# Kernel tuning notes

Hardware: AMD Instinct MI355X
Metric: run time of the kernel (lower is better)

Reference implementation:

```python
import jax, jax.numpy as jnp
import numpy as np

D_MODEL = 1024
D_STATE = 64


def setup_inputs() -> dict:
    key = jax.random.key(0)
    k_x, k_a, k_b, k_c, k_d = jax.random.split(key, 5)
    x = jax.random.normal(k_x, (4, 4096, D_MODEL), dtype=jnp.float32)
    # parameter init mirrors _init_parameters
    A_diag = jax.random.uniform(k_a, (D_STATE,), minval=-0.5, maxval=0.5, dtype=jnp.float32)
    def xavier(k, shape):
        fan_in, fan_out = shape
        limit = float(np.sqrt(6.0 / (fan_in + fan_out)))
        return jax.random.uniform(k, shape, minval=-limit, maxval=limit, dtype=jnp.float32)
    B = xavier(k_b, (D_MODEL, D_STATE))
    C = xavier(k_c, (D_STATE, D_MODEL))
    D = xavier(k_d, (D_MODEL, D_MODEL)) * 0.1
    return {"x": x, "A_diag": A_diag, "B": B, "C": C, "D": D}


def reference(x, A_diag, B, C, D):
    # h_t = sigmoid(A_diag) * h_{t-1} + x_t @ B ; y_t = h_t @ C + x_t @ D
    # dropout is identity in eval mode.
    a = jax.nn.sigmoid(A_diag)                      # [S_state]
    u = jnp.einsum('btd,ds->bts', x, B)             # precompute input drive [B,T,S]

    def step(h, u_t):                               # h: [B,S], u_t: [B,S]
        h = a * h + u_t
        return h, h

    h0 = jnp.zeros((x.shape[0], A_diag.shape[0]), dtype=x.dtype)
    _, hs = jax.lax.scan(step, h0, jnp.swapaxes(u, 0, 1))  # hs: [T,B,S]
    hs = jnp.swapaxes(hs, 0, 1)                            # [B,T,S]
    y = jnp.einsum('bts,sd->btd', hs, C) + jnp.einsum('btd,de->bte', x, D)
    return y
```

## Files before the change

kernel.cpp:

```cpp
#include <hip/hip_runtime.h>
#include <hip/hip_bf16.h>

using bf16x8 = __attribute__((ext_vector_type(8))) __bf16;
using f32x4  = __attribute__((ext_vector_type(4))) float;

#define MTOT   16384
#define DMODEL 1024
#define DSTATE 64
#define KBIG   1088

__device__ __forceinline__ ushort f2b(float f) {
  __hip_bfloat16 h = __float2bfloat16(f);
  return *reinterpret_cast<ushort*>(&h);
}

__device__ __forceinline__ void gld_lds16(const ushort* g, const char* l) {
  using gptr_t = const __attribute__((address_space(1))) uint32_t*;
  using lptr_t = __attribute__((address_space(3))) uint32_t*;
  __builtin_amdgcn_global_load_lds(
      reinterpret_cast<gptr_t>(reinterpret_cast<uintptr_t>(g)),
      reinterpret_cast<lptr_t>(static_cast<uint32_t>(reinterpret_cast<uintptr_t>(l))),
      16, 0, 0);
}

#define BARRIER() do { asm volatile("" ::: "memory"); __builtin_amdgcn_s_barrier(); asm volatile("" ::: "memory"); } while (0)
#define VMCNT4() asm volatile("s_waitcnt vmcnt(4)" ::: "memory")
#define VMCNT0() asm volatile("s_waitcnt vmcnt(0)" ::: "memory")

__global__ __launch_bounds__(256) void prep_wb(const float* __restrict__ A_diag,
    const float* __restrict__ B, const float* __restrict__ C, const float* __restrict__ D,
    ushort* __restrict__ Wt, ushort* __restrict__ Btu, float* __restrict__ aSig) {
  __shared__ float tile[64][65];
  int bid = blockIdx.x;
  int tid = threadIdx.x;
  int r = tid >> 2;
  if (bid < 272) {
    int bk = bid % 17, bn = bid / 17;
    int k0 = bk * 64, n0 = bn * 64;
    const float* srow = (k0 + r < DSTATE)
        ? (C + (size_t)(k0 + r) * DMODEL + n0)
        : (D + (size_t)(k0 + r - DSTATE) * DMODEL + n0);
#pragma unroll
    for (int it = 0; it < 4; ++it) {
      int c4 = (tid & 3) + it * 4;
      float4 v = *reinterpret_cast<const float4*>(srow + c4 * 4);
      tile[r][c4 * 4 + 0] = v.x; tile[r][c4 * 4 + 1] = v.y;
      tile[r][c4 * 4 + 2] = v.z; tile[r][c4 * 4 + 3] = v.w;
    }
    __syncthreads();
#pragma unroll
    for (int it = 0; it < 2; ++it) {
      int gq = (tid & 3) + it * 4;
      ushort o[8];
#pragma unroll
      for (int j = 0; j < 8; ++j) o[j] = f2b(tile[gq * 8 + j][r]);
      *reinterpret_cast<uint4*>(&Wt[(size_t)(n0 + r) * KBIG + k0 + gq * 8]) =
          *reinterpret_cast<uint4*>(o);
    }
  } else {
    int k0 = (bid - 272) * 64;
    const float* srow = B + (size_t)(k0 + r) * DSTATE;
#pragma unroll
    for (int it = 0; it < 4; ++it) {
      int c4 = (tid & 3) + it * 4;
      float4 v = *reinterpret_cast<const float4*>(srow + c4 * 4);
      tile[r][c4 * 4 + 0] = v.x; tile[r][c4 * 4 + 1] = v.y;
      tile[r][c4 * 4 + 2] = v.z; tile[r][c4 * 4 + 3] = v.w;
    }
    __syncthreads();
#pragma unroll
    for (int it = 0; it < 2; ++it) {
      int gq = (tid & 3) + it * 4;
      ushort o[8];
#pragma unroll
      for (int j = 0; j < 8; ++j) o[j] = f2b(tile[gq * 8 + j][r]);
      *reinterpret_cast<uint4*>(&Btu[(size_t)r * DMODEL + k0 + gq * 8]) =
          *reinterpret_cast<uint4*>(o);
    }
    if (bid == 272 && tid < DSTATE) aSig[tid] = 1.0f / (1.0f + expf(-A_diag[tid]));
  }
}

__global__ __launch_bounds__(256) void fused_xu(const float* __restrict__ x,
    const ushort* __restrict__ Btu, const float* __restrict__ aSig,
    ushort* __restrict__ Z, float* __restrict__ Uloc, float* __restrict__ carry) {
  __shared__ ushort As[64][136];
  __shared__ float  Ul[64][68];
  int tid = threadIdx.x;
  int w = tid >> 6, lane = tid & 63;
  int l16 = lane & 15, lh = lane >> 4;
  int row0 = blockIdx.x * 64;

  f32x4 acc[4] = {};
  float4 xv[4][2];
#pragma unroll
  for (int p = 0; p < 4; ++p) {
    int fi = p * 256 + tid;
    int r = fi >> 4, kq = fi & 15;
    const float* src = x + (size_t)(row0 + r) * 1024 + kq * 8;
    xv[p][0] = *reinterpret_cast<const float4*>(src);
    xv[p][1] = *reinterpret_cast<const float4*>(src + 4);
  }
  for (int c = 0; c < 8; ++c) {
    int k0 = c * 128;
#pragma unroll
    for (int p = 0; p < 4; ++p) {
      int fi = p * 256 + tid;
      int r = fi >> 4, kq = fi & 15;
      ushort o[8] = {f2b(xv[p][0].x), f2b(xv[p][0].y), f2b(xv[p][0].z), f2b(xv[p][0].w),
                     f2b(xv[p][1].x), f2b(xv[p][1].y), f2b(xv[p][1].z), f2b(xv[p][1].w)};
      uint4 pk = *reinterpret_cast<uint4*>(o);
      *reinterpret_cast<uint4*>(&Z[(size_t)(row0 + r) * KBIG + DSTATE + k0 + kq * 8]) = pk;
      *reinterpret_cast<uint4*>(&As[r][kq * 8]) = pk;
    }
    __syncthreads();
    if (c < 7) {
      int k1 = k0 + 128;
#pragma unroll
      for (int p = 0; p < 4; ++p) {
        int fi = p * 256 + tid;
        int r = fi >> 4, kq = fi & 15;
        const float* src = x + (size_t)(row0 + r) * 1024 + k1 + kq * 8;
        xv[p][0] = *reinterpret_cast<const float4*>(src);
        xv[p][1] = *reinterpret_cast<const float4*>(src + 4);
      }
    }
#pragma unroll
    for (int ks = 0; ks < 4; ++ks) {
      bf16x8 af = *reinterpret_cast<const bf16x8*>(&As[w * 16 + l16][ks * 32 + lh * 8]);
#pragma unroll
      for (int n = 0; n < 4; ++n) {
        bf16x8 bf = *reinterpret_cast<const bf16x8*>(
            &Btu[(size_t)(n * 16 + l16) * 1024 + k0 + ks * 32 + lh * 8]);
        acc[n] = __builtin_amdgcn_mfma_f32_16x16x32_bf16(af, bf, acc[n], 0, 0, 0);
      }
    }
    __syncthreads();
  }
#pragma unroll
  for (int n = 0; n < 4; ++n)
#pragma unroll
    for (int j = 0; j < 4; ++j)
      Ul[w * 16 + lh * 4 + j][n * 16 + l16] = acc[n][j];
  __syncthreads();
  int s = lane;
  float as = aSig[s];
  float h = 0.0f;
  int g = blockIdx.x * 4 + w;
#pragma unroll
  for (int i = 0; i < 16; ++i) {
    h = fmaf(as, h, Ul[w * 16 + i][s]);
    Uloc[(size_t)(g * 16 + i) * 64 + s] = h;
  }
  carry[(size_t)g * 64 + s] = h;
}

__global__ __launch_bounds__(256) void scan_fix2(const float* __restrict__ aSig,
    const float* __restrict__ Uloc, const float* __restrict__ carry,
    ushort* __restrict__ Z) {
  int w = threadIdx.x >> 6, s = threadIdx.x & 63;
  int g = blockIdx.x * 4 + w;
  int b = g >> 8, c = g & 255;
  float as = aSig[s];
  float aL = as;
#pragma unroll
  for (int q = 0; q < 4; ++q) aL *= aL;
  const float* cb = carry + ((size_t)b << 8) * 64 + s;
  float H = 0.0f;
  for (int c0 = 0; c0 < 256; c0 += 16) {
    if (c0 >= c) break;
    float v[16];
#pragma unroll
    for (int i = 0; i < 16; ++i) v[i] = cb[(size_t)(c0 + i) * 64];
#pragma unroll
    for (int i = 0; i < 16; ++i)
      if (c0 + i < c) H = fmaf(aL, H, v[i]);
  }
  float p = as;
  size_t ubase = (size_t)g * 16 * 64 + s;
  size_t zbase = (size_t)(g * 16) * KBIG + s;
#pragma unroll
  for (int i = 0; i < 16; ++i) {
    float h = fmaf(p, H, Uloc[ubase + (size_t)i * 64]);
    p *= as;
    Z[zbase + (size_t)i * KBIG] = f2b(h);
  }
}

__global__ __launch_bounds__(512) void gemm256(const ushort* __restrict__ A, int lda,
                                               const ushort* __restrict__ Bt, int ldb,
                                               float* __restrict__ Cc, int ldc, int K) {
  extern __shared__ __align__(128) char smem[];
  const int tid = threadIdx.x;
  const int wid = tid >> 6, lane = tid & 63;
  const int wm = wid >> 2, wn = wid & 3;
  const int l16 = lane & 15, lh = lane >> 4;

  int bid = blockIdx.x;
  int swz = (bid & 7) * ((int)gridDim.x >> 3) + (bid >> 3);
  const int bmRow = (swz >> 2) * 256;
  const int bnCol = (swz & 3) * 256;

  const int NT = K / 64;

  const int cswz = ((lh ^ (l16 & 7)) << 4);
  const int sRow = lane >> 3;
  const int sCol = (((lane & 7) ^ (lane >> 3)) << 3);

  f32x4 acc[8][4] = {};
  bf16x8 aR[8], bR[8];

  auto stageA = [&](int buf, int t, int h) {
    size_t r = (size_t)(bmRow + h * 128 + wid * 8 + sRow);
    const ushort* g0 = A + r * (size_t)lda + t * 64 + sCol;
    const char* d = smem + buf * 65536 + (h * 128 + wid * 8) * 128;
    gld_lds16(g0, d);
    gld_lds16(g0 + (size_t)64 * lda, d + 64 * 128);
  };
  auto stageB = [&](int buf, int t, int h) {
    size_t r = (size_t)(bnCol + h * 128 + wid * 8 + sRow);
    const ushort* g0 = Bt + r * (size_t)ldb + t * 64 + sCol;
    const char* d = smem + buf * 65536 + 32768 + (h * 128 + wid * 8) * 128;
    gld_lds16(g0, d);
    gld_lds16(g0 + (size_t)64 * ldb, d + 64 * 128);
  };
  auto loadA = [&](int buf, int qm) {
#pragma unroll
    for (int m = 0; m < 4; ++m)
#pragma unroll
      for (int ks = 0; ks < 2; ++ks)
        aR[m * 2 + ks] = *reinterpret_cast<const bf16x8*>(
            smem + buf * 65536 + (wm * 128 + qm * 64 + m * 16 + l16) * 128 + (cswz ^ (ks * 64)));
  };
  auto loadB = [&](int buf, int qn) {
#pragma unroll
    for (int n = 0; n < 2; ++n)
#pragma unroll
      for (int ks = 0; ks < 2; ++ks)
        bR[qn * 4 + n * 2 + ks] = *reinterpret_cast<const bf16x8*>(
            smem + buf * 65536 + 32768 + (wn * 64 + qn * 32 + n * 16 + l16) * 128 + (cswz ^ (ks * 64)));
  };
  auto mfmaQ = [&](int qm, int qn) {
    __builtin_amdgcn_s_setprio(1);
    __builtin_amdgcn_sched_barrier(0);
#pragma unroll
    for (int ks = 0; ks < 2; ++ks)
#pragma unroll
      for (int m = 0; m < 4; ++m)
#pragma unroll
        for (int n = 0; n < 2; ++n)
          acc[qm * 4 + m][qn * 2 + n] = __builtin_amdgcn_mfma_f32_16x16x32_bf16(
              aR[m * 2 + ks], bR[qn * 4 + n * 2 + ks], acc[qm * 4 + m][qn * 2 + n], 0, 0, 0);
    __builtin_amdgcn_sched_barrier(0);
    __builtin_amdgcn_s_setprio(0);
  };

  stageA(0, 0, 0); stageA(0, 0, 1); stageB(0, 0, 0); stageB(0, 0, 1);
  if (1 < NT) { stageA(1, 1, 0); stageA(1, 1, 1); stageB(1, 1, 0); stageB(1, 1, 1); }
  VMCNT0();
  BARRIER();

  for (int t = 0; t < NT; t += 2) {
    const bool s01 = (t > 0) && (t + 1 < NT);
    const bool s23 = (t + 2 < NT);
    const bool s67 = (t + 3 < NT);
    loadA(0, 0); loadB(0, 0);
    if (s01) stageA(1, t + 1, 0);
    BARRIER(); mfmaQ(0, 0); BARRIER();
    loadB(0, 1);
    if (s01) stageA(1, t + 1, 1);
    BARRIER(); mfmaQ(0, 1); BARRIER();
    loadA(0, 1);
    if (s23) stageB(0, t + 2, 0);
    BARRIER(); mfmaQ(1, 0); BARRIER();
    if (s23) stageB(0, t + 2, 1);
    BARRIER(); mfmaQ(1, 1);
    if (s23) { VMCNT4(); } else { VMCNT0(); }
    BARRIER();
    if (t + 1 < NT) {
      loadA(1, 0); loadB(1, 0);
      if (s23) stageA(0, t + 2, 0);
      BARRIER(); mfmaQ(0, 0); BARRIER();
      loadB(1, 1);
      if (s23) stageA(0, t + 2, 1);
      BARRIER(); mfmaQ(0, 1); BARRIER();
      loadA(1, 1);
      if (s67) stageB(1, t + 3, 0);
      BARRIER(); mfmaQ(1, 0); BARRIER();
      if (s67) stageB(1, t + 3, 1);
      BARRIER(); mfmaQ(1, 1);
      if (s67) { VMCNT4(); } else { VMCNT0(); }
      BARRIER();
    }
  }

#pragma unroll
  for (int i = 0; i < 8; ++i)
#pragma unroll
    for (int jn = 0; jn < 4; ++jn)
#pragma unroll
      for (int j = 0; j < 4; ++j) {
        int r = bmRow + wm * 128 + (i >> 2) * 64 + (i & 3) * 16 + lh * 4 + j;
        int c = bnCol + wn * 64 + (jn >> 1) * 32 + (jn & 1) * 16 + l16;
        Cc[(size_t)r * ldc + c] = acc[i][jn][j];
      }
}

extern "C" void kernel_launch(void* const* d_in, const int* in_sizes, int n_in,
                              void* d_out, int out_size, void* d_ws, size_t ws_size,
                              hipStream_t stream) {
  const float* x      = (const float*)d_in[0];
  const float* A_diag = (const float*)d_in[1];
  const float* B      = (const float*)d_in[2];
  const float* C      = (const float*)d_in[3];
  const float* D      = (const float*)d_in[4];
  float* y = (float*)d_out;

  char* w = (char*)d_ws;
  ushort* Z     = (ushort*)(w);
  ushort* Wt    = (ushort*)(w + 35651584);
  ushort* Btu   = (ushort*)(w + 37879808);
  float*  Uloc  = (float*) (w + 38010880);
  float*  carry = (float*) (w + 42205184);
  float*  aSig  = (float*) (w + 42467328);

  (void)hipFuncSetAttribute(reinterpret_cast<const void*>(&gemm256),
                            hipFuncAttributeMaxDynamicSharedMemorySize, 131072);

  prep_wb<<<dim3(288), dim3(256), 0, stream>>>(A_diag, B, C, D, Wt, Btu, aSig);
  fused_xu<<<dim3(256), dim3(256), 0, stream>>>(x, Btu, aSig, Z, Uloc, carry);
  scan_fix2<<<dim3(256), dim3(256), 0, stream>>>(aSig, Uloc, carry, Z);
  gemm256<<<dim3(64 * 4), dim3(512), 131072, stream>>>(Z, KBIG, Wt, KBIG, y, DMODEL, KBIG);
}
```

Measured before the change: 84.85 us.

## Fuse weight prep, input projection and chunked scan into one cooperative kernel

Merges the three pre-GEMM kernels (weight transpose/convert, x@B with local scan, and scan fix-up) into a single cooperative kernel that uses grid-wide syncs between phases. Local chunk states stay in shared memory across the second grid sync, so the Uloc global round trip is removed. The intent is to cut two kernel launch gaps and the Uloc write and read traffic. In exchange it relies on cooperative launch with all 256 blocks co-resident and adds grid-barrier overhead.

```diff
diff --git a/kernel.cpp b/kernel.cpp
--- a/kernel.cpp
+++ b/kernel.cpp
@@ -1,5 +1,8 @@
 #include <hip/hip_runtime.h>
 #include <hip/hip_bf16.h>
+#include <hip/hip_cooperative_groups.h>
+
+namespace cg = cooperative_groups;
 
 using bf16x8 = __attribute__((ext_vector_type(8))) __bf16;
 using f32x4  = __attribute__((ext_vector_type(4))) float;
@@ -27,163 +30,162 @@
 #define VMCNT4() asm volatile("s_waitcnt vmcnt(4)" ::: "memory")
 #define VMCNT0() asm volatile("s_waitcnt vmcnt(0)" ::: "memory")
 
-__global__ __launch_bounds__(256) void prep_wb(const float* __restrict__ A_diag,
-    const float* __restrict__ B, const float* __restrict__ C, const float* __restrict__ D,
-    ushort* __restrict__ Wt, ushort* __restrict__ Btu, float* __restrict__ aSig) {
-  __shared__ float tile[64][65];
-  int bid = blockIdx.x;
-  int tid = threadIdx.x;
-  int r = tid >> 2;
-  if (bid < 272) {
-    int bk = bid % 17, bn = bid / 17;
-    int k0 = bk * 64, n0 = bn * 64;
-    const float* srow = (k0 + r < DSTATE)
-        ? (C + (size_t)(k0 + r) * DMODEL + n0)
-        : (D + (size_t)(k0 + r - DSTATE) * DMODEL + n0);
-#pragma unroll
-    for (int it = 0; it < 4; ++it) {
-      int c4 = (tid & 3) + it * 4;
-      float4 v = *reinterpret_cast<const float4*>(srow + c4 * 4);
-      tile[r][c4 * 4 + 0] = v.x; tile[r][c4 * 4 + 1] = v.y;
-      tile[r][c4 * 4 + 2] = v.z; tile[r][c4 * 4 + 3] = v.w;
-    }
-    __syncthreads();
-#pragma unroll
-    for (int it = 0; it < 2; ++it) {
-      int gq = (tid & 3) + it * 4;
-      ushort o[8];
-#pragma unroll
-      for (int j = 0; j < 8; ++j) o[j] = f2b(tile[gq * 8 + j][r]);
-      *reinterpret_cast<uint4*>(&Wt[(size_t)(n0 + r) * KBIG + k0 + gq * 8]) =
-          *reinterpret_cast<uint4*>(o);
-    }
-  } else {
-    int k0 = (bid - 272) * 64;
-    const float* srow = B + (size_t)(k0 + r) * DSTATE;
-#pragma unroll
-    for (int it = 0; it < 4; ++it) {
-      int c4 = (tid & 3) + it * 4;
-      float4 v = *reinterpret_cast<const float4*>(srow + c4 * 4);
-      tile[r][c4 * 4 + 0] = v.x; tile[r][c4 * 4 + 1] = v.y;
-      tile[r][c4 * 4 + 2] = v.z; tile[r][c4 * 4 + 3] = v.w;
-    }
-    __syncthreads();
-#pragma unroll
-    for (int it = 0; it < 2; ++it) {
-      int gq = (tid & 3) + it * 4;
-      ushort o[8];
-#pragma unroll
-      for (int j = 0; j < 8; ++j) o[j] = f2b(tile[gq * 8 + j][r]);
-      *reinterpret_cast<uint4*>(&Btu[(size_t)r * DMODEL + k0 + gq * 8]) =
-          *reinterpret_cast<uint4*>(o);
-    }
-    if (bid == 272 && tid < DSTATE) aSig[tid] = 1.0f / (1.0f + expf(-A_diag[tid]));
+__global__ __launch_bounds__(256) void mega(const float* __restrict__ x,
+    const float* __restrict__ A_diag, const float* __restrict__ B,
+    const float* __restrict__ C, const float* __restrict__ D,
+    ushort* __restrict__ Wt, ushort* __restrict__ Btu, float* __restrict__ aSig,
+    ushort* __restrict__ Z, float* __restrict__ carry) {
+  __shared__ __align__(16) char smem_u[34816];
+  float  (*tile)[65] = reinterpret_cast<float(*)[65]>(smem_u);
+  ushort (*As)[136]  = reinterpret_cast<ushort(*)[136]>(smem_u);
+  float  (*Ul)[68]   = reinterpret_cast<float(*)[68]>(smem_u + 17408);
+
+  const int tid = threadIdx.x;
+  const int w = tid >> 6, lane = tid & 63;
+  const int l16 = lane & 15, lh = lane >> 4;
+
+  if (blockIdx.x == 0 && tid < DSTATE) aSig[tid] = 1.0f / (1.0f + expf(-A_diag[tid]));
+  {
+    int r = tid >> 2;
+    for (int job = blockIdx.x; job < 288; job += 256) {
+      if (job < 272) {
+        int bk = job % 17, bn = job / 17;
+        int k0 = bk * 64, n0 = bn * 64;
+        const float* srow = (k0 + r < DSTATE)
+            ? (C + (size_t)(k0 + r) * DMODEL + n0)
+            : (D + (size_t)(k0 + r - DSTATE) * DMODEL + n0);
+#pragma unroll
+        for (int it = 0; it < 4; ++it) {
+          int c4 = (tid & 3) + it * 4;
+          float4 v = *reinterpret_cast<const float4*>(srow + c4 * 4);
+          tile[r][c4 * 4 + 0] = v.x; tile[r][c4 * 4 + 1] = v.y;
+          tile[r][c4 * 4 + 2] = v.z; tile[r][c4 * 4 + 3] = v.w;
+        }
+        __syncthreads();
+#pragma unroll
+        for (int it = 0; it < 2; ++it) {
+          int gq = (tid & 3) + it * 4;
+          ushort o[8];
+#pragma unroll
+          for (int j = 0; j < 8; ++j) o[j] = f2b(tile[gq * 8 + j][r]);
+          *reinterpret_cast<uint4*>(&Wt[(size_t)(n0 + r) * KBIG + k0 + gq * 8]) =
+              *reinterpret_cast<uint4*>(o);
+        }
+      } else {
+        int k0 = (job - 272) * 64;
+        const float* srow = B + (size_t)(k0 + r) * DSTATE;
+#pragma unroll
+        for (int it = 0; it < 4; ++it) {
+          int c4 = (tid & 3) + it * 4;
+          float4 v = *reinterpret_cast<const float4*>(srow + c4 * 4);
+          tile[r][c4 * 4 + 0] = v.x; tile[r][c4 * 4 + 1] = v.y;
+          tile[r][c4 * 4 + 2] = v.z; tile[r][c4 * 4 + 3] = v.w;
+        }
+        __syncthreads();
+#pragma unroll
+        for (int it = 0; it < 2; ++it) {
+          int gq = (tid & 3) + it * 4;
+          ushort o[8];
+#pragma unroll
+          for (int j = 0; j < 8; ++j) o[j] = f2b(tile[gq * 8 + j][r]);
+          *reinterpret_cast<uint4*>(&Btu[(size_t)r * DMODEL + k0 + gq * 8]) =
+              *reinterpret_cast<uint4*>(o);
+        }
+      }
+      __syncthreads();
+    }
   }
-}
-
-__global__ __launch_bounds__(256) void fused_xu(const float* __restrict__ x,
-    const ushort* __restrict__ Btu, const float* __restrict__ aSig,
-    ushort* __restrict__ Z, float* __restrict__ Uloc, float* __restrict__ carry) {
-  __shared__ ushort As[64][136];
-  __shared__ float  Ul[64][68];
-  int tid = threadIdx.x;
-  int w = tid >> 6, lane = tid & 63;
-  int l16 = lane & 15, lh = lane >> 4;
-  int row0 = blockIdx.x * 64;
-
-  f32x4 acc[4] = {};
-  float4 xv[4][2];
-#pragma unroll
-  for (int p = 0; p < 4; ++p) {
-    int fi = p * 256 + tid;
-    int r = fi >> 4, kq = fi & 15;
-    const float* src = x + (size_t)(row0 + r) * 1024 + kq * 8;
-    xv[p][0] = *reinterpret_cast<const float4*>(src);
-    xv[p][1] = *reinterpret_cast<const float4*>(src + 4);
-  }
-  for (int c = 0; c < 8; ++c) {
-    int k0 = c * 128;
+
+  cg::this_grid().sync();
+
+  const int row0 = blockIdx.x * 64;
+  const int g = blockIdx.x * 4 + w;
+  {
+    f32x4 acc[4] = {};
+    float4 xv[4][2];
 #pragma unroll
     for (int p = 0; p < 4; ++p) {
       int fi = p * 256 + tid;
       int r = fi >> 4, kq = fi & 15;
-      ushort o[8] = {f2b(xv[p][0].x), f2b(xv[p][0].y), f2b(xv[p][0].z), f2b(xv[p][0].w),
-                     f2b(xv[p][1].x), f2b(xv[p][1].y), f2b(xv[p][1].z), f2b(xv[p][1].w)};
-      uint4 pk = *reinterpret_cast<uint4*>(o);
-      *reinterpret_cast<uint4*>(&Z[(size_t)(row0 + r) * KBIG + DSTATE + k0 + kq * 8]) = pk;
-      *reinterpret_cast<uint4*>(&As[r][kq * 8]) = pk;
-    }
-    __syncthreads();
-    if (c < 7) {
-      int k1 = k0 + 128;
+      const float* src = x + (size_t)(row0 + r) * 1024 + kq * 8;
+      xv[p][0] = *reinterpret_cast<const float4*>(src);
+      xv[p][1] = *reinterpret_cast<const float4*>(src + 4);
+    }
+    for (int c = 0; c < 8; ++c) {
+      int k0 = c * 128;
 #pragma unroll
       for (int p = 0; p < 4; ++p) {
         int fi = p * 256 + tid;
         int r = fi >> 4, kq = fi & 15;
-        const float* src = x + (size_t)(row0 + r) * 1024 + k1 + kq * 8;
-        xv[p][0] = *reinterpret_cast<const float4*>(src);
-        xv[p][1] = *reinterpret_cast<const float4*>(src + 4);
-      }
-    }
-#pragma unroll
-    for (int ks = 0; ks < 4; ++ks) {
-      bf16x8 af = *reinterpret_cast<const bf16x8*>(&As[w * 16 + l16][ks * 32 + lh * 8]);
-#pragma unroll
-      for (int n = 0; n < 4; ++n) {
-        bf16x8 bf = *reinterpret_cast<const bf16x8*>(
-            &Btu[(size_t)(n * 16 + l16) * 1024 + k0 + ks * 32 + lh * 8]);
-        acc[n] = __builtin_amdgcn_mfma_f32_16x16x32_bf16(af, bf, acc[n], 0, 0, 0);
-      }
-    }
-    __syncthreads();
+        ushort o[8] = {f2b(xv[p][0].x), f2b(xv[p][0].y), f2b(xv[p][0].z), f2b(xv[p][0].w),
+                       f2b(xv[p][1].x), f2b(xv[p][1].y), f2b(xv[p][1].z), f2b(xv[p][1].w)};
+        uint4 pk = *reinterpret_cast<uint4*>(o);
+        *reinterpret_cast<uint4*>(&Z[(size_t)(row0 + r) * KBIG + DSTATE + k0 + kq * 8]) = pk;
+        *reinterpret_cast<uint4*>(&As[r][kq * 8]) = pk;
+      }
+      __syncthreads();
+      if (c < 7) {
+        int k1 = k0 + 128;
+#pragma unroll
+        for (int p = 0; p < 4; ++p) {
+          int fi = p * 256 + tid;
+          int r = fi >> 4, kq = fi & 15;
+          const float* src = x + (size_t)(row0 + r) * 1024 + k1 + kq * 8;
+          xv[p][0] = *reinterpret_cast<const float4*>(src);
+          xv[p][1] = *reinterpret_cast<const float4*>(src + 4);
+        }
+      }
+#pragma unroll
+      for (int ks = 0; ks < 4; ++ks) {
+        bf16x8 af = *reinterpret_cast<const bf16x8*>(&As[w * 16 + l16][ks * 32 + lh * 8]);
+#pragma unroll
+        for (int n = 0; n < 4; ++n) {
+          bf16x8 bf = *reinterpret_cast<const bf16x8*>(
+              &Btu[(size_t)(n * 16 + l16) * 1024 + k0 + ks * 32 + lh * 8]);
+          acc[n] = __builtin_amdgcn_mfma_f32_16x16x32_bf16(af, bf, acc[n], 0, 0, 0);
+        }
+      }
+      __syncthreads();
+    }
+#pragma unroll
+    for (int n = 0; n < 4; ++n)
+#pragma unroll
+      for (int j = 0; j < 4; ++j)
+        Ul[w * 16 + lh * 4 + j][n * 16 + l16] = acc[n][j];
+    float as = aSig[lane];
+    float h = 0.0f;
+#pragma unroll
+    for (int i = 0; i < 16; ++i) h = fmaf(as, h, Ul[w * 16 + i][lane]);
+    carry[(size_t)g * 64 + lane] = h;
   }
-#pragma unroll
-  for (int n = 0; n < 4; ++n)
-#pragma unroll
-    for (int j = 0; j < 4; ++j)
-      Ul[w * 16 + lh * 4 + j][n * 16 + l16] = acc[n][j];
-  __syncthreads();
-  int s = lane;
-  float as = aSig[s];
-  float h = 0.0f;
-  int g = blockIdx.x * 4 + w;
-#pragma unroll
-  for (int i = 0; i < 16; ++i) {
-    h = fmaf(as, h, Ul[w * 16 + i][s]);
-    Uloc[(size_t)(g * 16 + i) * 64 + s] = h;
-  }
-  carry[(size_t)g * 64 + s] = h;
-}
-
-__global__ __launch_bounds__(256) void scan_fix2(const float* __restrict__ aSig,
-    const float* __restrict__ Uloc, const float* __restrict__ carry,
-    ushort* __restrict__ Z) {
-  int w = threadIdx.x >> 6, s = threadIdx.x & 63;
-  int g = blockIdx.x * 4 + w;
-  int b = g >> 8, c = g & 255;
-  float as = aSig[s];
-  float aL = as;
-#pragma unroll
-  for (int q = 0; q < 4; ++q) aL *= aL;
-  const float* cb = carry + ((size_t)b << 8) * 64 + s;
-  float H = 0.0f;
-  for (int c0 = 0; c0 < 256; c0 += 16) {
-    if (c0 >= c) break;
-    float v[16];
-#pragma unroll
-    for (int i = 0; i < 16; ++i) v[i] = cb[(size_t)(c0 + i) * 64];
-#pragma unroll
-    for (int i = 0; i < 16; ++i)
-      if (c0 + i < c) H = fmaf(aL, H, v[i]);
-  }
-  float p = as;
-  size_t ubase = (size_t)g * 16 * 64 + s;
-  size_t zbase = (size_t)(g * 16) * KBIG + s;
-#pragma unroll
-  for (int i = 0; i < 16; ++i) {
-    float h = fmaf(p, H, Uloc[ubase + (size_t)i * 64]);
-    p *= as;
-    Z[zbase + (size_t)i * KBIG] = f2b(h);
+
+  __threadfence();
+  cg::this_grid().sync();
+
+  {
+    int b = g >> 8, c = g & 255;
+    float as = aSig[lane];
+    float aL = as;
+#pragma unroll
+    for (int q = 0; q < 4; ++q) aL *= aL;
+    const float* cb = carry + ((size_t)b << 8) * 64 + lane;
+    float H = 0.0f;
+    for (int c0 = 0; c0 < 256; c0 += 16) {
+      if (c0 >= c) break;
+      float v[16];
+#pragma unroll
+      for (int i = 0; i < 16; ++i) v[i] = cb[(size_t)(c0 + i) * 64];
+#pragma unroll
+      for (int i = 0; i < 16; ++i)
+        if (c0 + i < c) H = fmaf(aL, H, v[i]);
+    }
+    float h = H;
+    size_t zbase = (size_t)(g * 16) * KBIG + lane;
+#pragma unroll
+    for (int i = 0; i < 16; ++i) {
+      h = fmaf(as, h, Ul[w * 16 + i][lane]);
+      Z[zbase + (size_t)i * KBIG] = f2b(h);
+    }
   }
 }
 
@@ -320,15 +322,15 @@
   ushort* Z     = (ushort*)(w);
   ushort* Wt    = (ushort*)(w + 35651584);
   ushort* Btu   = (ushort*)(w + 37879808);
-  float*  Uloc  = (float*) (w + 38010880);
-  float*  carry = (float*) (w + 42205184);
-  float*  aSig  = (float*) (w + 42467328);
+  float*  carry = (float*) (w + 38010880);
+  float*  aSig  = (float*) (w + 38273024);
 
   (void)hipFuncSetAttribute(reinterpret_cast<const void*>(&gemm256),
                             hipFuncAttributeMaxDynamicSharedMemorySize, 131072);
 
-  prep_wb<<<dim3(288), dim3(256), 0, stream>>>(A_diag, B, C, D, Wt, Btu, aSig);
-  fused_xu<<<dim3(256), dim3(256), 0, stream>>>(x, Btu, aSig, Z, Uloc, carry);
-  scan_fix2<<<dim3(256), dim3(256), 0, stream>>>(aSig, Uloc, carry, Z);
+  void* args[] = {(void*)&x, (void*)&A_diag, (void*)&B, (void*)&C, (void*)&D,
+                  (void*)&Wt, (void*)&Btu, (void*)&aSig, (void*)&Z, (void*)&carry};
+  (void)hipLaunchCooperativeKernel(reinterpret_cast<void*>(&mega),
+                                   dim3(256), dim3(256), args, 0, stream);
   gemm256<<<dim3(64 * 4), dim3(512), 131072, stream>>>(Z, KBIG, Wt, KBIG, y, DMODEL, KBIG);
 }
```

Result: slower. 182.2 us (+114.8%).

## Replace 256x256 GEMM tile with 128x128 tile and simpler double-buffered loop

Applied to the files above, without the earlier changes.

The output GEMM moves from 256x256 block tiles (256 blocks, 128KB LDS) to 128x128 tiles (1024 blocks, 64KB LDS), with per-wave 64x32 sub-tiles. The quarter-split, heavily barriered schedule is replaced by a plain one-tile-per-iteration double buffer that prefetches two tiles ahead. The aim is more resident blocks per CU and better load balance to hide memory latency. In exchange, data reuse per block drops, so more global/L2 traffic and more LDS reads per MFMA.

```diff
diff --git a/kernel.cpp b/kernel.cpp
--- a/kernel.cpp
+++ b/kernel.cpp
@@ -187,9 +187,9 @@
   }
 }
 
-__global__ __launch_bounds__(512) void gemm256(const ushort* __restrict__ A, int lda,
-                                               const ushort* __restrict__ Bt, int ldb,
-                                               float* __restrict__ Cc, int ldc, int K) {
+__global__ __launch_bounds__(512, 4) void gemm128(const ushort* __restrict__ A, int lda,
+                                                  const ushort* __restrict__ Bt, int ldb,
+                                                  float* __restrict__ Cc, int ldc, int K) {
   extern __shared__ __align__(128) char smem[];
   const int tid = threadIdx.x;
   const int wid = tid >> 6, lane = tid & 63;
@@ -198,111 +198,83 @@
 
   int bid = blockIdx.x;
   int swz = (bid & 7) * ((int)gridDim.x >> 3) + (bid >> 3);
-  const int bmRow = (swz >> 2) * 256;
-  const int bnCol = (swz & 3) * 256;
-
+  const int bmRow = (swz >> 3) * 128;
+  const int bnCol = (swz & 7) * 128;
   const int NT = K / 64;
 
   const int cswz = ((lh ^ (l16 & 7)) << 4);
   const int sRow = lane >> 3;
   const int sCol = (((lane & 7) ^ (lane >> 3)) << 3);
 
-  f32x4 acc[8][4] = {};
-  bf16x8 aR[8], bR[8];
-
-  auto stageA = [&](int buf, int t, int h) {
-    size_t r = (size_t)(bmRow + h * 128 + wid * 8 + sRow);
-    const ushort* g0 = A + r * (size_t)lda + t * 64 + sCol;
-    const char* d = smem + buf * 65536 + (h * 128 + wid * 8) * 128;
-    gld_lds16(g0, d);
-    gld_lds16(g0 + (size_t)64 * lda, d + 64 * 128);
+  const ushort* aBase = A + (size_t)(bmRow + wid * 8 + sRow) * lda + sCol;
+  const ushort* bBase = Bt + (size_t)(bnCol + wid * 8 + sRow) * ldb + sCol;
+
+  f32x4 acc[4][2] = {};
+  bf16x8 aR[8], bR[4];
+
+  auto stageA = [&](int buf, int t) {
+    const ushort* g = aBase + (size_t)t * 64;
+    char* d = smem + buf * 32768 + (wid * 8) * 128;
+    gld_lds16(g, d);
+    gld_lds16(g + (size_t)64 * lda, d + 64 * 128);
   };
-  auto stageB = [&](int buf, int t, int h) {
-    size_t r = (size_t)(bnCol + h * 128 + wid * 8 + sRow);
-    const ushort* g0 = Bt + r * (size_t)ldb + t * 64 + sCol;
-    const char* d = smem + buf * 65536 + 32768 + (h * 128 + wid * 8) * 128;
-    gld_lds16(g0, d);
-    gld_lds16(g0 + (size_t)64 * ldb, d + 64 * 128);
+  auto stageB = [&](int buf, int t) {
+    const ushort* g = bBase + (size_t)t * 64;
+    char* d = smem + buf * 32768 + 16384 + (wid * 8) * 128;
+    gld_lds16(g, d);
+    gld_lds16(g + (size_t)64 * ldb, d + 64 * 128);
   };
-  auto loadA = [&](int buf, int qm) {
+  auto readA = [&](int buf) {
 #pragma unroll
     for (int m = 0; m < 4; ++m)
 #pragma unroll
       for (int ks = 0; ks < 2; ++ks)
         aR[m * 2 + ks] = *reinterpret_cast<const bf16x8*>(
-            smem + buf * 65536 + (wm * 128 + qm * 64 + m * 16 + l16) * 128 + (cswz ^ (ks * 64)));
+            smem + buf * 32768 + (wm * 64 + m * 16 + l16) * 128 + (cswz ^ (ks * 64)));
   };
-  auto loadB = [&](int buf, int qn) {
+  auto readB = [&](int buf) {
 #pragma unroll
     for (int n = 0; n < 2; ++n)
 #pragma unroll
       for (int ks = 0; ks < 2; ++ks)
-        bR[qn * 4 + n * 2 + ks] = *reinterpret_cast<const bf16x8*>(
-            smem + buf * 65536 + 32768 + (wn * 64 + qn * 32 + n * 16 + l16) * 128 + (cswz ^ (ks * 64)));
+        bR[n * 2 + ks] = *reinterpret_cast<const bf16x8*>(
+            smem + buf * 32768 + 16384 + (wn * 32 + n * 16 + l16) * 128 + (cswz ^ (ks * 64)));
   };
-  auto mfmaQ = [&](int qm, int qn) {
+
+  stageA(0, 0); stageB(0, 0);
+  stageA(1, 1); stageB(1, 1);
+  VMCNT4();
+  BARRIER();
+
+  for (int t = 0; t < NT; ++t) {
+    const int buf = t & 1;
+    const bool st2 = (t + 2 < NT);
+    readA(buf); readB(buf);
+    BARRIER();
+    if (st2) { stageA(buf, t + 2); stageB(buf, t + 2); }
     __builtin_amdgcn_s_setprio(1);
-    __builtin_amdgcn_sched_barrier(0);
 #pragma unroll
     for (int ks = 0; ks < 2; ++ks)
 #pragma unroll
       for (int m = 0; m < 4; ++m)
 #pragma unroll
         for (int n = 0; n < 2; ++n)
-          acc[qm * 4 + m][qn * 2 + n] = __builtin_amdgcn_mfma_f32_16x16x32_bf16(
-              aR[m * 2 + ks], bR[qn * 4 + n * 2 + ks], acc[qm * 4 + m][qn * 2 + n], 0, 0, 0);
-    __builtin_amdgcn_sched_barrier(0);
+          acc[m][n] = __builtin_amdgcn_mfma_f32_16x16x32_bf16(
+              aR[m * 2 + ks], bR[n * 2 + ks], acc[m][n], 0, 0, 0);
     __builtin_amdgcn_s_setprio(0);
-  };
-
-  stageA(0, 0, 0); stageA(0, 0, 1); stageB(0, 0, 0); stageB(0, 0, 1);
-  if (1 < NT) { stageA(1, 1, 0); stageA(1, 1, 1); stageB(1, 1, 0); stageB(1, 1, 1); }
-  VMCNT0();
-  BARRIER();
-
-  for (int t = 0; t < NT; t += 2) {
-    const bool s01 = (t > 0) && (t + 1 < NT);
-    const bool s23 = (t + 2 < NT);
-    const bool s67 = (t + 3 < NT);
-    loadA(0, 0); loadB(0, 0);
-    if (s01) stageA(1, t + 1, 0);
-    BARRIER(); mfmaQ(0, 0); BARRIER();
-    loadB(0, 1);
-    if (s01) stageA(1, t + 1, 1);
-    BARRIER(); mfmaQ(0, 1); BARRIER();
-    loadA(0, 1);
-    if (s23) stageB(0, t + 2, 0);
-    BARRIER(); mfmaQ(1, 0); BARRIER();
-    if (s23) stageB(0, t + 2, 1);
-    BARRIER(); mfmaQ(1, 1);
-    if (s23) { VMCNT4(); } else { VMCNT0(); }
+    if (st2) { VMCNT4(); } else { VMCNT0(); }
     BARRIER();
-    if (t + 1 < NT) {
-      loadA(1, 0); loadB(1, 0);
-      if (s23) stageA(0, t + 2, 0);
-      BARRIER(); mfmaQ(0, 0); BARRIER();
-      loadB(1, 1);
-      if (s23) stageA(0, t + 2, 1);
-      BARRIER(); mfmaQ(0, 1); BARRIER();
-      loadA(1, 1);
-      if (s67) stageB(1, t + 3, 0);
-      BARRIER(); mfmaQ(1, 0); BARRIER();
-      if (s67) stageB(1, t + 3, 1);
-      BARRIER(); mfmaQ(1, 1);
-      if (s67) { VMCNT4(); } else { VMCNT0(); }
-      BARRIER();
-    }
-  }
-
-#pragma unroll
-  for (int i = 0; i < 8; ++i)
-#pragma unroll
-    for (int jn = 0; jn < 4; ++jn)
+  }
+
+#pragma unroll
+  for (int m = 0; m < 4; ++m)
+#pragma unroll
+    for (int n = 0; n < 2; ++n)
 #pragma unroll
       for (int j = 0; j < 4; ++j) {
-        int r = bmRow + wm * 128 + (i >> 2) * 64 + (i & 3) * 16 + lh * 4 + j;
-        int c = bnCol + wn * 64 + (jn >> 1) * 32 + (jn & 1) * 16 + l16;
-        Cc[(size_t)r * ldc + c] = acc[i][jn][j];
+        int r = bmRow + wm * 64 + m * 16 + lh * 4 + j;
+        int c = bnCol + wn * 32 + n * 16 + l16;
+        Cc[(size_t)r * ldc + c] = acc[m][n][j];
       }
 }
 
@@ -324,11 +296,11 @@
   float*  carry = (float*) (w + 42205184);
   float*  aSig  = (float*) (w + 42467328);
 
-  (void)hipFuncSetAttribute(reinterpret_cast<const void*>(&gemm256),
-                            hipFuncAttributeMaxDynamicSharedMemorySize, 131072);
+  (void)hipFuncSetAttribute(reinterpret_cast<const void*>(&gemm128),
+                            hipFuncAttributeMaxDynamicSharedMemorySize, 65536);
 
   prep_wb<<<dim3(288), dim3(256), 0, stream>>>(A_diag, B, C, D, Wt, Btu, aSig);
   fused_xu<<<dim3(256), dim3(256), 0, stream>>>(x, Btu, aSig, Z, Uloc, carry);
   scan_fix2<<<dim3(256), dim3(256), 0, stream>>>(aSig, Uloc, carry, Z);
-  gemm256<<<dim3(64 * 4), dim3(512), 131072, stream>>>(Z, KBIG, Wt, KBIG, y, DMODEL, KBIG);
-}
+  gemm128<<<dim3(128 * 8), dim3(512), 65536, stream>>>(Z, KBIG, Wt, KBIG, y, DMODEL, KBIG);
+}
```

Measured after the change: 86.32 us. Within noise of the previous version (+1.7%).
